# Performance work log

Hardware: AMD Instinct MI355X
Metric: run time of the kernel (lower is better)

The kernel has to match this reference:

```python
import jax, jax.numpy as jnp
import numpy as np

N, E, S, G = 20000, 60000, 3000, 128
EAD = 5
DIMS = [(16, 32), (32, 64), (64, 64)]  # NNConv (M_in, M_out) per layer
HID = 128  # edge-MLP hidden
FC_IN = 64 + 8  # conv output + raw continuous feats


def setup_inputs() -> dict:
    key = jax.random.key(0)
    ks = iter(jax.random.split(key, 64))
    inp = {}
    inp['x'] = jax.random.normal(next(ks), (N, 24), jnp.float32)
    inp['edge_index'] = jax.random.randint(next(ks), (2, E), 0, N)
    inp['edge_attr'] = jax.random.uniform(next(ks), (E, EAD), jnp.float32)
    inp['node_to_subgraph'] = jnp.sort(jax.random.randint(next(ks), (N,), 0, S))
    inp['subgraph_to_graph'] = jnp.sort(jax.random.randint(next(ks), (S,), 0, G))
    for i, (mi, mo) in enumerate(DIMS):
        inp[f'conv{i}_w1'] = jax.random.normal(next(ks), (EAD, HID), jnp.float32) / np.sqrt(EAD)
        inp[f'conv{i}_b1'] = jnp.zeros((HID,), jnp.float32)
        inp[f'conv{i}_w2'] = jax.random.normal(next(ks), (HID, mi * mo), jnp.float32) / np.sqrt(HID * mi)
        inp[f'conv{i}_b2'] = jnp.zeros((mi * mo,), jnp.float32)
        inp[f'conv{i}_root'] = jax.random.normal(next(ks), (mi, mo), jnp.float32) / np.sqrt(mi)
        inp[f'conv{i}_bias'] = jnp.zeros((mo,), jnp.float32)
    dims_fc = [(FC_IN, FC_IN // 2), (FC_IN // 2, FC_IN // 4), (FC_IN // 4, 1)]
    for i, (di, do) in enumerate(dims_fc):
        inp[f'fc{i+1}_w'] = jax.random.normal(next(ks), (di, do), jnp.float32) / np.sqrt(di)
        inp[f'fc{i+1}_b'] = jnp.zeros((do,), jnp.float32)
    return inp


def _nnconv(x, src, dst, ea, w1, b1, w2, b2, root, bias):
    # edge MLP -> per-edge weight matrix [E, M_in, M_out]
    h = jax.nn.relu(ea @ w1 + b1)
    mi, mo = root.shape
    W = (h @ w2 + b2).reshape(-1, mi, mo)
    msg = jnp.einsum('ei,eio->eo', x[src], W)  # gather + per-edge matmul
    agg = jax.ops.segment_sum(msg, dst, num_segments=x.shape[0])  # scatter-add
    return agg + x @ root + bias


def _mean_pool(x, seg, num):
    s = jax.ops.segment_sum(x, seg, num_segments=num)
    c = jax.ops.segment_sum(jnp.ones((x.shape[0], 1), x.dtype), seg, num_segments=num)
    return s / jnp.maximum(c, 1.0)


def _forward(x, edge_index, edge_attr, node_to_subgraph, subgraph_to_graph, convs, fcs):
    src, dst = edge_index[0], edge_index[1]
    xi = x[:, :16]
    for p in convs:
        xi = jax.nn.elu(_nnconv(xi, src, dst, edge_attr, *p))
    x_cont = x[:, 16:]
    xc = jnp.concatenate([xi, x_cont], axis=1)  # [N, 72]
    xs = _mean_pool(xc, node_to_subgraph, S)    # [S, 72]
    xg = _mean_pool(xs, subgraph_to_graph, G)   # [G, 72]
    (w1, b1), (w2, b2), (w3, b3) = fcs
    xg = jax.nn.elu(xg @ w1 + b1)
    xg = jax.nn.elu(xg @ w2 + b2)
    return (xg @ w3 + b3).reshape(-1)


def reference(x, edge_index, edge_attr, node_to_subgraph, subgraph_to_graph,
              conv0_w1, conv0_b1, conv0_w2, conv0_b2, conv0_root, conv0_bias,
              conv1_w1, conv1_b1, conv1_w2, conv1_b2, conv1_root, conv1_bias,
              conv2_w1, conv2_b1, conv2_w2, conv2_b2, conv2_root, conv2_bias,
              fc1_w, fc1_b, fc2_w, fc2_b, fc3_w, fc3_b):
    convs = [
        (conv0_w1, conv0_b1, conv0_w2, conv0_b2, conv0_root, conv0_bias),
        (conv1_w1, conv1_b1, conv1_w2, conv1_b2, conv1_root, conv1_bias),
        (conv2_w1, conv2_b1, conv2_w2, conv2_b2, conv2_root, conv2_bias),
    ]
    fcs = [(fc1_w, fc1_b), (fc2_w, fc2_b), (fc3_w, fc3_b)]
    return _forward(x, edge_index, edge_attr, node_to_subgraph, subgraph_to_graph, convs, fcs)
```

## Files before the change

### kernel.cpp

```cpp
#include <hip/hip_runtime.h>
#include <hip/hip_bf16.h>
#include <cmath>

#define NN 20000
#define NE 60000
#define NS 3000
#define NG 128
#define HIDN 128
#define SCB 79
#define TILES 938
#define SLST 3840000

typedef float f32x16 __attribute__((ext_vector_type(16)));
typedef _Float16 f16x8 __attribute__((ext_vector_type(8)));

__device__ __forceinline__ float eluf(float v) { return v > 0.f ? v : expm1f(v); }

__device__ __forceinline__ void gload_lds16(const void* g, void* l) {
    __builtin_amdgcn_global_load_lds(
        (const __attribute__((address_space(1))) unsigned int*)g,
        (__attribute__((address_space(3))) unsigned int*)l, 16, 0, 0);
}

__device__ __forceinline__ void vmwait0() {
    asm volatile("s_waitcnt vmcnt(0)" ::: "memory");
}
__device__ __forceinline__ void vmwait8() {
    asm volatile("s_waitcnt vmcnt(8)" ::: "memory");
}

__global__ void k_hist(const int* __restrict__ dst, int* __restrict__ deg) {
    int e = blockIdx.x * 256 + threadIdx.x;
    if (e < NE) atomicAdd(&deg[dst[e]], 1);
}

__global__ void k_scan1(const int* __restrict__ deg, int* __restrict__ bsum) {
    __shared__ int s[256];
    const int t = threadIdx.x;
    int i = blockIdx.x * 256 + t;
    s[t] = (i < NN) ? deg[i] : 0;
    __syncthreads();
#pragma unroll
    for (int off = 128; off > 0; off >>= 1) {
        if (t < off) s[t] += s[t + off];
        __syncthreads();
    }
    if (t == 0) bsum[blockIdx.x] = s[0];
}

__global__ void k_scan2(const int* __restrict__ bsum, int* __restrict__ boff) {
    __shared__ int s[SCB];
    const int t = threadIdx.x;
    if (t < SCB) s[t] = bsum[t];
    __syncthreads();
    if (t == 0) {
        int acc = 0;
        for (int i = 0; i < SCB; ++i) { int v = s[i]; s[i] = acc; acc += v; }
    }
    __syncthreads();
    if (t < SCB) boff[t] = s[t];
}

__global__ void k_scan3(const int* __restrict__ deg, const int* __restrict__ boff,
                        int* __restrict__ rowptr) {
    __shared__ int s[256];
    const int t = threadIdx.x;
    int i = blockIdx.x * 256 + t;
    int v = (i < NN) ? deg[i] : 0;
    s[t] = v;
    __syncthreads();
#pragma unroll
    for (int off = 1; off < 256; off <<= 1) {
        int a = (t >= off) ? s[t - off] : 0;
        __syncthreads();
        s[t] += a;
        __syncthreads();
    }
    if (i < NN) rowptr[i + 1] = boff[blockIdx.x] + s[t];
    if (i == 0) rowptr[0] = 0;
}

__global__ void k_scatter(const int* __restrict__ src, const int* __restrict__ dst,
                          const int* __restrict__ rowptr, int* __restrict__ tmp,
                          int* __restrict__ eord, int* __restrict__ srcS) {
    int e = blockIdx.x * 256 + threadIdx.x;
    if (e >= NE) return;
    int d = dst[e];
    int pos = rowptr[d] + atomicAdd(&tmp[d], 1);
    eord[pos] = e;
    srcS[pos] = src[e];
}

#define PRE_N0 66048
#define PRE_N1 264192
#define PRE_N2 528384
#define PRE_N3 320000
#define PRE_TOT (PRE_N0 + PRE_N1 + PRE_N2 + PRE_N3)

__global__ void k_prep(const float* __restrict__ w20, const float* __restrict__ b20,
                       const float* __restrict__ w21, const float* __restrict__ b21,
                       const float* __restrict__ w22, const float* __restrict__ b22,
                       const float* __restrict__ x,
                       _Float16* __restrict__ w2t0, _Float16* __restrict__ w2t1,
                       _Float16* __restrict__ w2t2, _Float16* __restrict__ x16h) {
    int idx = blockIdx.x * 256 + threadIdx.x;
    if (idx < PRE_N0) {
        constexpr int KP = 129 * 16, KF = 128 * 16, MO = 32;
        int o = idx / KP, kg = idx % KP;
        float v = (kg < KF) ? w20[(size_t)kg * MO + o] : b20[(kg - KF) * MO + o];
        w2t0[idx] = (_Float16)v;
    } else if (idx < PRE_N0 + PRE_N1) {
        int i2 = idx - PRE_N0;
        constexpr int KP = 129 * 32, KF = 128 * 32, MO = 64;
        int o = i2 / KP, kg = i2 % KP;
        float v = (kg < KF) ? w21[(size_t)kg * MO + o] : b21[(kg - KF) * MO + o];
        w2t1[i2] = (_Float16)v;
    } else if (idx < PRE_N0 + PRE_N1 + PRE_N2) {
        int i2 = idx - PRE_N0 - PRE_N1;
        constexpr int KP = 129 * 64, KF = 128 * 64, MO = 64;
        int o = i2 / KP, kg = i2 % KP;
        float v = (kg < KF) ? w22[(size_t)kg * MO + o] : b22[(kg - KF) * MO + o];
        w2t2[i2] = (_Float16)v;
    } else if (idx < PRE_TOT) {
        int i2 = idx - PRE_N0 - PRE_N1 - PRE_N2;
        int n = i2 >> 4, i = i2 & 15;
        x16h[i2] = (_Float16)x[n * 24 + i];
    }
}

template <int MI, int MO, int XS>
__global__ __launch_bounds__(256, 2) void k_edgeB(
    const _Float16* __restrict__ xi, const float* __restrict__ ea,
    const float* __restrict__ w1, const float* __restrict__ b1,
    const _Float16* __restrict__ w2t, const int* __restrict__ srcS,
    const int* __restrict__ eord, _Float16* __restrict__ msg) {
    constexpr int PH  = MI / 16;
    constexpr int KP  = 129 * MI;
    constexpr int NT  = MO / 32;
    constexpr int CH  = 16 / (PH * NT);
    constexpr int NCH = 64 / CH;
    static_assert(CH * PH * NT == 16, "ITEMS must be 16");

    __shared__ __align__(16) _Float16 sb[2][2][16 * 512];

    const int lane = threadIdx.x & 63;
    const int w    = threadIdx.x >> 6;
    const int mg   = w & 1;
    const int kh   = w >> 1;
    const int lo5  = lane & 31;
    const int hi   = lane >> 5;
    const int e0   = blockIdx.x * 128 + mg * 64;
    const int kb   = kh * 64;

    const int rc0 = min(e0 + lo5, NE - 1);
    const int rc1 = min(e0 + 32 + lo5, NE - 1);
    const int s0 = srcS[rc0];
    const int s1 = srcS[rc1];

    float ea0[5], ea1[5];
    {
        const int eo0 = eord[rc0], eo1 = eord[rc1];
#pragma unroll
        for (int d = 0; d < 5; ++d) {
            ea0[d] = ea[eo0 * 5 + d];
            ea1[d] = ea[eo1 * 5 + d];
        }
    }

    f16x8 xr0[PH], xr1[PH];
    {
        const _Float16* xb0 = xi + (size_t)s0 * XS + hi * 8;
        const _Float16* xb1 = xi + (size_t)s1 * XS + hi * 8;
#pragma unroll
        for (int p = 0; p < PH; ++p) {
            xr0[p] = *reinterpret_cast<const f16x8*>(xb0 + p * 16);
            xr1[p] = *reinterpret_cast<const f16x8*>(xb1 + p * 16);
        }
    }

    f32x16 acc[2][NT];
#pragma unroll
    for (int m = 0; m < 2; ++m)
#pragma unroll
        for (int n = 0; n < NT; ++n)
#pragma unroll
            for (int i = 0; i < 16; ++i) acc[m][n][i] = 0.f;

    auto stage = [&](int buf, int kc) {
#pragma unroll
        for (int jj = 0; jj < 8; ++jj) {
            const int j  = mg + jj * 2;
            const int n  = j % NT;
            const int kp = j / NT;
            const int p  = kp % PH;
            const int kk = kp / PH;
            gload_lds16(w2t + (size_t)(n * 32 + lo5) * KP
                            + (size_t)(kb + kc + kk) * MI + p * 16 + hi * 8,
                        &sb[kh][buf][j * 512]);
        }
    };

    auto calc_h = [&](int kc, _Float16* h0, _Float16* h1) {
#pragma unroll
        for (int kk = 0; kk < CH; ++kk) {
            const int k = kb + kc + kk;
            const float c0 = w1[0 * HIDN + k], c1 = w1[1 * HIDN + k],
                        c2 = w1[2 * HIDN + k], c3 = w1[3 * HIDN + k],
                        c4 = w1[4 * HIDN + k], bb = b1[k];
            float t0 = bb, t1 = bb;
            t0 = fmaf(ea0[0], c0, t0); t1 = fmaf(ea1[0], c0, t1);
            t0 = fmaf(ea0[1], c1, t0); t1 = fmaf(ea1[1], c1, t1);
            t0 = fmaf(ea0[2], c2, t0); t1 = fmaf(ea1[2], c2, t1);
            t0 = fmaf(ea0[3], c3, t0); t1 = fmaf(ea1[3], c3, t1);
            t0 = fmaf(ea0[4], c4, t0); t1 = fmaf(ea1[4], c4, t1);
            h0[kk] = (_Float16)fmaxf(t0, 0.f);
            h1[kk] = (_Float16)fmaxf(t1, 0.f);
        }
    };

    auto compute = [&](int buf, const _Float16* h0, const _Float16* h1) {
        const _Float16* sbc = &sb[kh][buf][0];
#pragma unroll
        for (int kk = 0; kk < CH; ++kk) {
            const _Float16 hv0 = h0[kk];
            const _Float16 hv1 = h1[kk];
            const f16x8 h80 = {hv0, hv0, hv0, hv0, hv0, hv0, hv0, hv0};
            const f16x8 h81 = {hv1, hv1, hv1, hv1, hv1, hv1, hv1, hv1};
#pragma unroll
            for (int p = 0; p < PH; ++p) {
                const f16x8 af0 = xr0[p] * h80;
                const f16x8 af1 = xr1[p] * h81;
#pragma unroll
                for (int n = 0; n < NT; ++n) {
                    const f16x8 bv = *reinterpret_cast<const f16x8*>(
                        &sbc[((kk * PH + p) * NT + n) * 512 + lane * 8]);
                    acc[0][n] = __builtin_amdgcn_mfma_f32_32x32x16_f16(af0, bv, acc[0][n], 0, 0, 0);
                    acc[1][n] = __builtin_amdgcn_mfma_f32_32x32x16_f16(af1, bv, acc[1][n], 0, 0, 0);
                }
            }
        }
    };

    _Float16 hA0[CH], hA1[CH], hB0[CH], hB1[CH];

    stage(0, 0);
    calc_h(0, hA0, hA1);

    for (int c = 0; c < NCH; c += 2) {
        stage(1, (c + 1) * CH);
        calc_h((c + 1) * CH, hB0, hB1);
        vmwait8();
        __builtin_amdgcn_sched_barrier(0);
        __builtin_amdgcn_s_barrier();
        __builtin_amdgcn_sched_barrier(0);
        compute(0, hA0, hA1);
        __builtin_amdgcn_sched_barrier(0);
        __builtin_amdgcn_s_barrier();

        const bool pf = (c + 2 < NCH);
        if (pf) {
            stage(0, (c + 2) * CH);
            calc_h((c + 2) * CH, hA0, hA1);
            vmwait8();
        } else {
            vmwait0();
        }
        __builtin_amdgcn_sched_barrier(0);
        __builtin_amdgcn_s_barrier();
        __builtin_amdgcn_sched_barrier(0);
        compute(1, hB0, hB1);
        __builtin_amdgcn_sched_barrier(0);
        __builtin_amdgcn_s_barrier();
    }

    if (kh == 1) {
#pragma unroll
        for (int p = 0; p < PH; ++p) {
#pragma unroll
            for (int n = 0; n < NT; ++n) {
                const f16x8 bv = *reinterpret_cast<const f16x8*>(
                    w2t + (size_t)(n * 32 + lo5) * KP + (size_t)128 * MI + p * 16 + hi * 8);
                acc[0][n] = __builtin_amdgcn_mfma_f32_32x32x16_f16(xr0[p], bv, acc[0][n], 0, 0, 0);
                acc[1][n] = __builtin_amdgcn_mfma_f32_32x32x16_f16(xr1[p], bv, acc[1][n], 0, 0, 0);
            }
        }
    }

    __syncthreads();
    float* red = reinterpret_cast<float*>(&sb[0][0][0]);
    if (kh == 1) {
#pragma unroll
        for (int m = 0; m < 2; ++m)
#pragma unroll
            for (int n = 0; n < NT; ++n) {
                float* d = red + (size_t)((mg * 2 + m) * NT + n) * 1024 + lane;
#pragma unroll
                for (int i = 0; i < 16; ++i) d[i * 64] = acc[m][n][i];
            }
    }
    __syncthreads();
    if (kh == 0) {
#pragma unroll
        for (int m = 0; m < 2; ++m)
#pragma unroll
            for (int n = 0; n < NT; ++n) {
                const float* s = red + (size_t)((mg * 2 + m) * NT + n) * 1024 + lane;
#pragma unroll
                for (int i = 0; i < 16; ++i) acc[m][n][i] += s[i * 64];
            }
#pragma unroll
        for (int m = 0; m < 2; ++m)
#pragma unroll
            for (int q = 0; q < 4; ++q)
#pragma unroll
                for (int a2 = 0; a2 < 4; ++a2) {
                    const int e = e0 + m * 32 + 4 * hi + 8 * q + a2;
                    if (e < NE) {
#pragma unroll
                        for (int n = 0; n < NT; ++n)
                            msg[(size_t)e * MO + n * 32 + lo5] =
                                (_Float16)acc[m][n][4 * q + a2];
                    }
                }
    }
}

template <int MI, int MO, int XS, int KSL, int NSL, int WV>
__global__ __launch_bounds__(WV * 64, WV / 4) void k_edgeP(
    const _Float16* __restrict__ xi, const float* __restrict__ ea,
    const float* __restrict__ w1, const float* __restrict__ b1,
    const _Float16* __restrict__ w2t, const int* __restrict__ srcS,
    const int* __restrict__ eord, _Float16* __restrict__ msgP, int tilesPerBlock) {
    constexpr int PH = MI / 16;
    constexpr int KP = 129 * MI;
    constexpr int NT = MO / 32;
    constexpr int LASTK = 129 - (NSL - 1) * KSL;
    constexpr int MAXITEMS = LASTK * PH * NT;

    __shared__ __align__(16) _Float16 sb[MAXITEMS * 512];

    const int t    = threadIdx.x;
    const int lane = t & 63;
    const int w    = t >> 6;
    const int lo5  = lane & 31;
    const int hi   = lane >> 5;

    const int sl    = blockIdx.y;
    const int k0    = sl * KSL;
    const int kspan = (sl == NSL - 1) ? LASTK : KSL;
    const int items = kspan * PH * NT;

    for (int j = w; j < items; j += WV) {
        const int kk  = j / (PH * NT);
        const int rem = j % (PH * NT);
        const int p   = rem / NT;
        const int n   = rem % NT;
        gload_lds16(w2t + (size_t)(n * 32 + lo5) * KP
                        + (size_t)(k0 + kk) * MI + p * 16 + hi * 8,
                    &sb[j * 512]);
    }
    vmwait0();
    __syncthreads();

    _Float16* msgS = msgP + (size_t)sl * ((size_t)NE * MO);
    const int tile0 = blockIdx.x * tilesPerBlock;
    const int tile1 = min(tile0 + tilesPerBlock, TILES);

    for (int tile = tile0 + w; tile < tile1; tile += WV) {
        const int e0  = tile * 64;
        const int rc0 = min(e0 + lo5, NE - 1);
        const int rc1 = min(e0 + 32 + lo5, NE - 1);
        const int s0 = srcS[rc0];
        const int s1 = srcS[rc1];

        float ea0[5], ea1[5];
        {
            const int eo0 = eord[rc0], eo1 = eord[rc1];
#pragma unroll
            for (int d = 0; d < 5; ++d) {
                ea0[d] = ea[eo0 * 5 + d];
                ea1[d] = ea[eo1 * 5 + d];
            }
        }

        f16x8 xr0[PH], xr1[PH];
        {
            const _Float16* xb0 = xi + (size_t)s0 * XS + hi * 8;
            const _Float16* xb1 = xi + (size_t)s1 * XS + hi * 8;
#pragma unroll
            for (int p = 0; p < PH; ++p) {
                xr0[p] = *reinterpret_cast<const f16x8*>(xb0 + p * 16);
                xr1[p] = *reinterpret_cast<const f16x8*>(xb1 + p * 16);
            }
        }

        f32x16 acc[2][NT];
#pragma unroll
        for (int m = 0; m < 2; ++m)
#pragma unroll
            for (int n = 0; n < NT; ++n)
#pragma unroll
                for (int i = 0; i < 16; ++i) acc[m][n][i] = 0.f;

        for (int kk2 = 0; kk2 < kspan; ++kk2) {
            const int k = k0 + kk2;
            _Float16 hv0, hv1;
            if (k < 128) {
                const float c0 = w1[0 * HIDN + k], c1 = w1[1 * HIDN + k],
                            c2 = w1[2 * HIDN + k], c3 = w1[3 * HIDN + k],
                            c4 = w1[4 * HIDN + k], bb = b1[k];
                float t0 = bb, t1 = bb;
                t0 = fmaf(ea0[0], c0, t0); t1 = fmaf(ea1[0], c0, t1);
                t0 = fmaf(ea0[1], c1, t0); t1 = fmaf(ea1[1], c1, t1);
                t0 = fmaf(ea0[2], c2, t0); t1 = fmaf(ea1[2], c2, t1);
                t0 = fmaf(ea0[3], c3, t0); t1 = fmaf(ea1[3], c3, t1);
                t0 = fmaf(ea0[4], c4, t0); t1 = fmaf(ea1[4], c4, t1);
                hv0 = (_Float16)fmaxf(t0, 0.f);
                hv1 = (_Float16)fmaxf(t1, 0.f);
            } else {
                hv0 = (_Float16)1.0f;
                hv1 = (_Float16)1.0f;
            }
            const f16x8 h80 = {hv0, hv0, hv0, hv0, hv0, hv0, hv0, hv0};
            const f16x8 h81 = {hv1, hv1, hv1, hv1, hv1, hv1, hv1, hv1};
#pragma unroll
            for (int p = 0; p < PH; ++p) {
                const f16x8 af0 = xr0[p] * h80;
                const f16x8 af1 = xr1[p] * h81;
#pragma unroll
                for (int n = 0; n < NT; ++n) {
                    const f16x8 bv = *reinterpret_cast<const f16x8*>(
                        &sb[((kk2 * PH + p) * NT + n) * 512 + lane * 8]);
                    acc[0][n] = __builtin_amdgcn_mfma_f32_32x32x16_f16(af0, bv, acc[0][n], 0, 0, 0);
                    acc[1][n] = __builtin_amdgcn_mfma_f32_32x32x16_f16(af1, bv, acc[1][n], 0, 0, 0);
                }
            }
        }

#pragma unroll
        for (int m = 0; m < 2; ++m)
#pragma unroll
            for (int q = 0; q < 4; ++q)
#pragma unroll
                for (int a2 = 0; a2 < 4; ++a2) {
                    const int e = e0 + m * 32 + 4 * hi + 8 * q + a2;
                    if (e < NE) {
#pragma unroll
                        for (int n = 0; n < NT; ++n)
                            msgS[(size_t)e * MO + n * 32 + lo5] =
                                (_Float16)acc[m][n][4 * q + a2];
                    }
                }
    }
}

template <int NSL>
__global__ void k_red(_Float16* __restrict__ msgP) {
    int idx = blockIdx.x * 256 + threadIdx.x;
    if (idx >= NE * 8) return;
    float a[8] = {0, 0, 0, 0, 0, 0, 0, 0};
#pragma unroll
    for (int sl = 0; sl < NSL; ++sl) {
        const f16x8 v = *reinterpret_cast<const f16x8*>(msgP + (size_t)sl * SLST + (size_t)idx * 8);
#pragma unroll
        for (int i = 0; i < 8; ++i) a[i] += (float)v[i];
    }
    f16x8 r;
#pragma unroll
    for (int i = 0; i < 8; ++i) r[i] = (_Float16)a[i];
    *reinterpret_cast<f16x8*>(msgP + (size_t)idx * 8) = r;
}

template <int MI, int MO, int XS>
__global__ void k_agg(const _Float16* __restrict__ msg, const int* __restrict__ rowptr,
                      const float* __restrict__ xi, const float* __restrict__ root,
                      const float* __restrict__ bias, float* __restrict__ out,
                      _Float16* __restrict__ outh) {
    int idx = blockIdx.x * 256 + threadIdx.x;
    if (idx >= NN * MO) return;
    int n = idx / MO, o = idx % MO;
    float s = bias[o];
#pragma unroll
    for (int i = 0; i < MI; ++i) s = fmaf(xi[(size_t)n * XS + i], root[i * MO + o], s);
    const int j0 = rowptr[n], j1 = rowptr[n + 1];
    for (int j = j0; j < j1; ++j) s += (float)msg[(size_t)j * MO + o];
    float r = eluf(s);
    out[idx] = r;
    outh[idx] = (_Float16)r;
}

__global__ void k_agg_pool(const _Float16* __restrict__ msg, const int* __restrict__ rowptr,
                           const float* __restrict__ xi, const float* __restrict__ root,
                           const float* __restrict__ bias, const float* __restrict__ x,
                           const int* __restrict__ n2s, float* __restrict__ xs_sum,
                           float* __restrict__ cs) {
    int idx = blockIdx.x * 256 + threadIdx.x;
    if (idx >= NN * 72) return;
    int n = idx / 72, o = idx % 72;
    float r;
    if (o < 64) {
        float s = bias[o];
#pragma unroll
        for (int i = 0; i < 64; ++i) s = fmaf(xi[(size_t)n * 64 + i], root[i * 64 + o], s);
        const int j0 = rowptr[n], j1 = rowptr[n + 1];
        for (int j = j0; j < j1; ++j) s += (float)msg[(size_t)j * 64 + o];
        r = eluf(s);
    } else {
        r = x[n * 24 + 16 + (o - 64)];
    }
    const int sg = n2s[n];
    atomicAdd(&xs_sum[sg * 72 + o], r);
    if (o == 0) atomicAdd(&cs[sg], 1.f);
}

__global__ void k_pool_g(const float* __restrict__ xs_sum, const float* __restrict__ cs,
                         const int* __restrict__ s2g, float* __restrict__ xg_sum,
                         float* __restrict__ cg) {
    int idx = blockIdx.x * 256 + threadIdx.x;
    if (idx >= NS * 72) return;
    int s = idx / 72, j = idx % 72;
    float v = xs_sum[s * 72 + j] / fmaxf(cs[s], 1.f);
    int g = s2g[s];
    atomicAdd(&xg_sum[g * 72 + j], v);
    if (j == 0) atomicAdd(&cg[g], 1.f);
}

__global__ void k_fc(const float* __restrict__ xg_sum, const float* __restrict__ cg,
                     const float* __restrict__ w1, const float* __restrict__ b1,
                     const float* __restrict__ w2, const float* __restrict__ b2,
                     const float* __restrict__ w3, const float* __restrict__ b3,
                     float* __restrict__ out) {
    int g = threadIdx.x;
    if (g >= NG) return;
    float inv = 1.f / fmaxf(cg[g], 1.f);
    float v[72];
#pragma unroll
    for (int j = 0; j < 72; ++j) v[j] = xg_sum[g * 72 + j] * inv;
    float h1[36];
#pragma unroll
    for (int o = 0; o < 36; ++o) {
        float s = b1[o];
#pragma unroll
        for (int i = 0; i < 72; ++i) s = fmaf(v[i], w1[i * 36 + o], s);
        h1[o] = eluf(s);
    }
    float h2[18];
#pragma unroll
    for (int o = 0; o < 18; ++o) {
        float s = b2[o];
#pragma unroll
        for (int i = 0; i < 36; ++i) s = fmaf(h1[i], w2[i * 18 + o], s);
        h2[o] = eluf(s);
    }
    float s = b3[0];
#pragma unroll
    for (int i = 0; i < 18; ++i) s = fmaf(h2[i], w3[i], s);
    out[g] = s;
}

extern "C" void kernel_launch(void* const* d_in, const int* in_sizes, int n_in,
                              void* d_out, int out_size, void* d_ws, size_t ws_size,
                              hipStream_t stream) {
    const float* x   = (const float*)d_in[0];
    const int*   ei  = (const int*)d_in[1];
    const float* ea  = (const float*)d_in[2];
    const int*   n2s = (const int*)d_in[3];
    const int*   s2g = (const int*)d_in[4];
    const int* src = ei;
    const int* dst = ei + NE;

    const float* cw1[3]   = {(const float*)d_in[5],  (const float*)d_in[11], (const float*)d_in[17]};
    const float* cb1[3]   = {(const float*)d_in[6],  (const float*)d_in[12], (const float*)d_in[18]};
    const float* cw2[3]   = {(const float*)d_in[7],  (const float*)d_in[13], (const float*)d_in[19]};
    const float* cb2[3]   = {(const float*)d_in[8],  (const float*)d_in[14], (const float*)d_in[20]};
    const float* croot[3] = {(const float*)d_in[9],  (const float*)d_in[15], (const float*)d_in[21]};
    const float* cbias[3] = {(const float*)d_in[10], (const float*)d_in[16], (const float*)d_in[22]};
    const float* fc1w = (const float*)d_in[23];
    const float* fc1b = (const float*)d_in[24];
    const float* fc2w = (const float*)d_in[25];
    const float* fc2b = (const float*)d_in[26];
    const float* fc3w = (const float*)d_in[27];
    const float* fc3b = (const float*)d_in[28];

    char* W = (char*)d_ws;
    float*    xiA   = (float*)(W);
    float*    xiB   = (float*)(W + 5120000);
    _Float16* xiAh  = (_Float16*)(W + 10240000);
    _Float16* xiBh  = (_Float16*)(W + 12800000);
    _Float16* x16h  = (_Float16*)(W + 15360000);
    float*    xs_sum= (float*)(W + 16000000);
    float*    cs    = (float*)(W + 16864000);
    float*    xg_sum= (float*)(W + 16876000);
    float*    cg    = (float*)(W + 16912864);
    int*      deg   = (int*)(W + 16913376);
    int*      tmp   = (int*)(W + 16993376);
    _Float16* w2t0  = (_Float16*)(W + 17073376);
    _Float16* w2t1  = (_Float16*)(W + 17205472);
    _Float16* w2t2  = (_Float16*)(W + 17733856);
    int*      rowptr= (int*)(W + 18790624);
    int*      eord  = (int*)(W + 18870640);
    int*      srcS  = (int*)(W + 19110640);
    int*      bsum  = (int*)(W + 19350640);
    int*      boff  = (int*)(W + 19350960);
    _Float16* msgP  = (_Float16*)(W + 19351296);
    const size_t NEED_P = 19351296ull + 8ull * 7680000ull;
    const bool useP = (ws_size >= NEED_P);
    _Float16* msg = msgP;

    hipMemsetAsync(xs_sum, 0, 1073376, stream);

    k_hist<<<(NE + 255) / 256, 256, 0, stream>>>(dst, deg);
    k_scan1<<<SCB, 256, 0, stream>>>(deg, bsum);
    k_scan2<<<1, 128, 0, stream>>>(bsum, boff);
    k_scan3<<<SCB, 256, 0, stream>>>(deg, boff, rowptr);
    k_scatter<<<(NE + 255) / 256, 256, 0, stream>>>(src, dst, rowptr, tmp, eord, srcS);

    k_prep<<<(PRE_TOT + 255) / 256, 256, 0, stream>>>(
        cw2[0], cb2[0], cw2[1], cb2[1], cw2[2], cb2[2], x, w2t0, w2t1, w2t2, x16h);

    const int EB = (NE + 127) / 128;
    const int REDB = (NE * 8 + 255) / 256;

    if (useP) {
        {
            const int XB = 118, TPB = 8;
            k_edgeP<16, 32, 16, 129, 1, 8><<<dim3(XB, 1), 512, 0, stream>>>(
                x16h, ea, cw1[0], cb1[0], w2t0, srcS, eord, msg, TPB);
        }
        k_agg<16, 32, 24><<<(NN * 32 + 255) / 256, 256, 0, stream>>>(msg, rowptr, x, croot[0], cbias[0], xiB, xiBh);

        {
            const int XB = 64, TPB = (TILES + 63) / 64;
            k_edgeP<32, 64, 32, 32, 4, 12><<<dim3(XB, 4), 768, 0, stream>>>(
                xiBh, ea, cw1[1], cb1[1], w2t1, srcS, eord, msgP, TPB);
        }
        k_red<4><<<REDB, 256, 0, stream>>>(msgP);
        k_agg<32, 64, 32><<<(NN * 64 + 255) / 256, 256, 0, stream>>>(msg, rowptr, xiB, croot[1], cbias[1], xiA, xiAh);

        {
            const int XB = 32, TPB = (TILES + 31) / 32;
            k_edgeP<64, 64, 64, 16, 8, 12><<<dim3(XB, 8), 768, 0, stream>>>(
                xiAh, ea, cw1[2], cb1[2], w2t2, srcS, eord, msgP, TPB);
        }
        k_red<8><<<REDB, 256, 0, stream>>>(msgP);
        k_agg_pool<<<(NN * 72 + 255) / 256, 256, 0, stream>>>(
            msg, rowptr, xiA, croot[2], cbias[2], x, n2s, xs_sum, cs);
    } else {
        k_edgeB<16, 32, 16><<<EB, 256, 0, stream>>>(x16h, ea, cw1[0], cb1[0], w2t0, srcS, eord, msg);
        k_agg<16, 32, 24><<<(NN * 32 + 255) / 256, 256, 0, stream>>>(msg, rowptr, x, croot[0], cbias[0], xiB, xiBh);
        k_edgeB<32, 64, 32><<<EB, 256, 0, stream>>>(xiBh, ea, cw1[1], cb1[1], w2t1, srcS, eord, msg);
        k_agg<32, 64, 32><<<(NN * 64 + 255) / 256, 256, 0, stream>>>(msg, rowptr, xiB, croot[1], cbias[1], xiA, xiAh);
        k_edgeB<64, 64, 64><<<EB, 256, 0, stream>>>(xiAh, ea, cw1[2], cb1[2], w2t2, srcS, eord, msg);
        k_agg_pool<<<(NN * 72 + 255) / 256, 256, 0, stream>>>(
            msg, rowptr, xiA, croot[2], cbias[2], x, n2s, xs_sum, cs);
    }

    k_pool_g<<<(NS * 72 + 255) / 256, 256, 0, stream>>>(xs_sum, cs, s2g, xg_sum, cg);
    k_fc<<<1, 128, 0, stream>>>(xg_sum, cg, fc1w, fc1b, fc2w, fc2b, fc3w, fc3b, (float*)d_out);
}
```

Baseline: 275.7 us.

## Split edge-MLP matmul over output columns as well as K to halve partial sums

The per-edge weight-generation matmul kernel now splits its grid dimension between K slices and 32-wide output-column halves, instead of splitting only along K. Each block handles one 32-column strip with fewer K slices, so the fp16 partial-message buffers and the following reduction pass shrink by half (2 slices instead of 4 for layer 1, 4 instead of 8 for layer 2). The cost is that each block recomputes the edge-MLP hidden activations and re-gathers source features for its column strip, and does fewer MFMAs per loaded A fragment.

```diff
diff --git a/kernel.cpp b/kernel.cpp
--- a/kernel.cpp
+++ b/kernel.cpp
@@ -325,7 +325,7 @@
     }
 }
 
-template <int MI, int MO, int XS, int KSL, int NSL, int WV>
+template <int MI, int MO, int XS, int KSL, int NKS, int NSP, int WV>
 __global__ __launch_bounds__(WV * 64, WV / 4) void k_edgeP(
     const _Float16* __restrict__ xi, const float* __restrict__ ea,
     const float* __restrict__ w1, const float* __restrict__ b1,
@@ -333,9 +333,8 @@
     const int* __restrict__ eord, _Float16* __restrict__ msgP, int tilesPerBlock) {
     constexpr int PH = MI / 16;
     constexpr int KP = 129 * MI;
-    constexpr int NT = MO / 32;
-    constexpr int LASTK = 129 - (NSL - 1) * KSL;
-    constexpr int MAXITEMS = LASTK * PH * NT;
+    constexpr int LASTK = 129 - (NKS - 1) * KSL;
+    constexpr int MAXITEMS = LASTK * PH;
 
     __shared__ __align__(16) _Float16 sb[MAXITEMS * 512];
 
@@ -346,23 +345,24 @@
     const int hi   = lane >> 5;
 
     const int sl    = blockIdx.y;
-    const int k0    = sl * KSL;
-    const int kspan = (sl == NSL - 1) ? LASTK : KSL;
-    const int items = kspan * PH * NT;
+    const int ksl   = sl / NSP;
+    const int nh    = sl % NSP;
+    const int k0    = ksl * KSL;
+    const int kspan = (ksl == NKS - 1) ? LASTK : KSL;
+    const int items = kspan * PH;
+    const int cb    = nh * 32;
 
     for (int j = w; j < items; j += WV) {
-        const int kk  = j / (PH * NT);
-        const int rem = j % (PH * NT);
-        const int p   = rem / NT;
-        const int n   = rem % NT;
-        gload_lds16(w2t + (size_t)(n * 32 + lo5) * KP
+        const int kk = j / PH;
+        const int p  = j % PH;
+        gload_lds16(w2t + (size_t)(cb + lo5) * KP
                         + (size_t)(k0 + kk) * MI + p * 16 + hi * 8,
                     &sb[j * 512]);
     }
     vmwait0();
     __syncthreads();
 
-    _Float16* msgS = msgP + (size_t)sl * ((size_t)NE * MO);
+    _Float16* msgS = msgP + (size_t)ksl * SLST;
     const int tile0 = blockIdx.x * tilesPerBlock;
     const int tile1 = min(tile0 + tilesPerBlock, TILES);
 
@@ -394,13 +394,9 @@
             }
         }
 
-        f32x16 acc[2][NT];
-#pragma unroll
-        for (int m = 0; m < 2; ++m)
-#pragma unroll
-            for (int n = 0; n < NT; ++n)
-#pragma unroll
-                for (int i = 0; i < 16; ++i) acc[m][n][i] = 0.f;
+        f32x16 acc0, acc1;
+#pragma unroll
+        for (int i = 0; i < 16; ++i) { acc0[i] = 0.f; acc1[i] = 0.f; }
 
         for (int kk2 = 0; kk2 < kspan; ++kk2) {
             const int k = k0 + kk2;
@@ -427,13 +423,10 @@
             for (int p = 0; p < PH; ++p) {
                 const f16x8 af0 = xr0[p] * h80;
                 const f16x8 af1 = xr1[p] * h81;
-#pragma unroll
-                for (int n = 0; n < NT; ++n) {
-                    const f16x8 bv = *reinterpret_cast<const f16x8*>(
-                        &sb[((kk2 * PH + p) * NT + n) * 512 + lane * 8]);
-                    acc[0][n] = __builtin_amdgcn_mfma_f32_32x32x16_f16(af0, bv, acc[0][n], 0, 0, 0);
-                    acc[1][n] = __builtin_amdgcn_mfma_f32_32x32x16_f16(af1, bv, acc[1][n], 0, 0, 0);
-                }
+                const f16x8 bv = *reinterpret_cast<const f16x8*>(
+                    &sb[(kk2 * PH + p) * 512 + lane * 8]);
+                acc0 = __builtin_amdgcn_mfma_f32_32x32x16_f16(af0, bv, acc0, 0, 0, 0);
+                acc1 = __builtin_amdgcn_mfma_f32_32x32x16_f16(af1, bv, acc1, 0, 0, 0);
             }
         }
 
@@ -445,22 +438,20 @@
                 for (int a2 = 0; a2 < 4; ++a2) {
                     const int e = e0 + m * 32 + 4 * hi + 8 * q + a2;
                     if (e < NE) {
-#pragma unroll
-                        for (int n = 0; n < NT; ++n)
-                            msgS[(size_t)e * MO + n * 32 + lo5] =
-                                (_Float16)acc[m][n][4 * q + a2];
+                        const float v = (m == 0) ? acc0[4 * q + a2] : acc1[4 * q + a2];
+                        msgS[(size_t)e * MO + cb + lo5] = (_Float16)v;
                     }
                 }
     }
 }
 
-template <int NSL>
+template <int NKS>
 __global__ void k_red(_Float16* __restrict__ msgP) {
     int idx = blockIdx.x * 256 + threadIdx.x;
     if (idx >= NE * 8) return;
     float a[8] = {0, 0, 0, 0, 0, 0, 0, 0};
 #pragma unroll
-    for (int sl = 0; sl < NSL; ++sl) {
+    for (int sl = 0; sl < NKS; ++sl) {
         const f16x8 v = *reinterpret_cast<const f16x8*>(msgP + (size_t)sl * SLST + (size_t)idx * 8);
 #pragma unroll
         for (int i = 0; i < 8; ++i) a[i] += (float)v[i];
@@ -603,7 +594,7 @@
     int*      bsum  = (int*)(W + 19350640);
     int*      boff  = (int*)(W + 19350960);
     _Float16* msgP  = (_Float16*)(W + 19351296);
-    const size_t NEED_P = 19351296ull + 8ull * 7680000ull;
+    const size_t NEED_P = 19351296ull + 4ull * 7680000ull;
     const bool useP = (ws_size >= NEED_P);
     _Float16* msg = msgP;
 
@@ -624,25 +615,25 @@
     if (useP) {
         {
             const int XB = 118, TPB = 8;
-            k_edgeP<16, 32, 16, 129, 1, 8><<<dim3(XB, 1), 512, 0, stream>>>(
+            k_edgeP<16, 32, 16, 129, 1, 1, 8><<<dim3(XB, 1), 512, 0, stream>>>(
                 x16h, ea, cw1[0], cb1[0], w2t0, srcS, eord, msg, TPB);
         }
         k_agg<16, 32, 24><<<(NN * 32 + 255) / 256, 256, 0, stream>>>(msg, rowptr, x, croot[0], cbias[0], xiB, xiBh);
 
         {
             const int XB = 64, TPB = (TILES + 63) / 64;
-            k_edgeP<32, 64, 32, 32, 4, 12><<<dim3(XB, 4), 768, 0, stream>>>(
+            k_edgeP<32, 64, 32, 64, 2, 2, 12><<<dim3(XB, 4), 768, 0, stream>>>(
                 xiBh, ea, cw1[1], cb1[1], w2t1, srcS, eord, msgP, TPB);
         }
-        k_red<4><<<REDB, 256, 0, stream>>>(msgP);
+        k_red<2><<<REDB, 256, 0, stream>>>(msgP);
         k_agg<32, 64, 32><<<(NN * 64 + 255) / 256, 256, 0, stream>>>(msg, rowptr, xiB, croot[1], cbias[1], xiA, xiAh);
 
         {
             const int XB = 32, TPB = (TILES + 31) / 32;
-            k_edgeP<64, 64, 64, 16, 8, 12><<<dim3(XB, 8), 768, 0, stream>>>(
+            k_edgeP<64, 64, 64, 32, 4, 2, 12><<<dim3(XB, 8), 768, 0, stream>>>(
                 xiAh, ea, cw1[2], cb1[2], w2t2, srcS, eord, msgP, TPB);
         }
-        k_red<8><<<REDB, 256, 0, stream>>>(msgP);
+        k_red<4><<<REDB, 256, 0, stream>>>(msgP);
         k_agg_pool<<<(NN * 72 + 255) / 256, 256, 0, stream>>>(
             msg, rowptr, xiA, croot[2], cbias[2], x, n2s, xs_sum, cs);
     } else {
```

Measured after the change: 276.8 us. No clear change (+0.4%).
